# Kernel optimization log

Measured on AMD Instinct MI355X. Metric: run time of the kernel, lower is better.

Reference implementation:

```python
import jax, jax.numpy as jnp
import numpy as np

NUM_HEADS = 12
KEEP_RATE = 0.7
INIT_N = 14 * 14  # 196


def setup_inputs() -> dict:
    key = jax.random.key(0)
    k1, k2, k3, k4 = jax.random.split(key, 4)
    B, N, C = 64, 197, 768
    s = 1.0 / np.sqrt(C)
    return {
        "x": jax.random.normal(k1, (B, N, C), dtype=jnp.float32),
        "qkv_w": jax.random.normal(k2, (3 * C, C), dtype=jnp.float32) * s,
        "proj_w": jax.random.normal(k3, (C, C), dtype=jnp.float32) * s,
        "proj_b": jax.random.normal(k4, (C,), dtype=jnp.float32) * 0.01,
    }


def reference(x, qkv_w, proj_w, proj_b):
    B, N, C = x.shape
    H = NUM_HEADS
    hd = C // H
    scale = hd ** (-0.5)

    # qkv projection (torch Linear: y = x @ W.T), split into q, k, v heads
    qkv = (x @ qkv_w.T).reshape(B, N, 3, H, hd)
    qkv = jnp.transpose(qkv, (2, 0, 3, 1, 4))  # [3, B, H, N, hd]
    q, k, v = qkv[0], qkv[1], qkv[2]

    # explicit (non-flash) attention: attn matrix is needed for cls-row pruning
    attn = jax.nn.softmax(jnp.einsum("bhqd,bhkd->bhqk", q, k) * scale, axis=-1)
    out = jnp.einsum("bhqk,bhkd->bqhd", attn, v).reshape(B, N, C)
    out = out @ proj_w.T + proj_b

    # top-k token pruning via mean cls attention over heads
    left_tokens = int(KEEP_RATE * INIT_N)  # 137
    cls_attn = attn[:, :, 0, 1:].mean(axis=1)  # [B, N-1]
    _, idx = jax.lax.top_k(cls_attn, left_tokens)  # sorted descending, like torch.topk
    index = jnp.broadcast_to(idx[:, :, None], (B, left_tokens, C))
    return (out, index, idx)
```

## Files before the change

kernel.cpp:

```cpp
#include <hip/hip_runtime.h>
#include <math.h>


typedef __attribute__((ext_vector_type(8))) short short8;
typedef __attribute__((ext_vector_type(4))) float f32x4;

constexpr int T_B = 64, T_N = 197, T_C = 768, T_H = 12, T_HD = 64;
constexpr int T_M = T_B * T_N;
constexpr int T_KEEP = 137, T_NTOK = 196;

constexpr size_t OOFF_INDEX = (size_t)T_M * T_C;
constexpr size_t OOFF_IDX   = OOFF_INDEX + (size_t)T_B * T_KEEP * T_C;

constexpr size_t U_XB_AO = 0;
constexpr size_t U_QWB   = 9682944;
constexpr size_t U_PWB   = 11452416;
constexpr size_t U_QB    = 12042240;
constexpr size_t U_KB    = 21725184;
constexpr size_t U_VB    = 31408128;
constexpr size_t WS_FP_BYTE = 82182144ull;

__device__ __forceinline__ float bf2f(short u) {
  return __builtin_bit_cast(float, ((unsigned)(unsigned short)u) << 16);
}
__device__ __forceinline__ unsigned short f2bf(float f) {
  unsigned u = __builtin_bit_cast(unsigned, f);
  return (unsigned short)((u + 0x7fffu + ((u >> 16) & 1u)) >> 16);
}

__global__ __launch_bounds__(256) void cvt_k(const float* __restrict__ in,
                                             unsigned short* __restrict__ outp)
{
  const int i = blockIdx.x * 256 + threadIdx.x;
  const float4 v = ((const float4*)in)[i];
  const unsigned long long pk =
      (unsigned long long)f2bf(v.x) | ((unsigned long long)f2bf(v.y) << 16) |
      ((unsigned long long)f2bf(v.z) << 32) | ((unsigned long long)f2bf(v.w) << 48);
  ((unsigned long long*)outp)[i] = pk;
}

__global__ __launch_bounds__(256) void vzero_k(unsigned short* __restrict__ vtg)
{
  const size_t i = ((size_t)blockIdx.x * 256 + threadIdx.x) * 8;
  *(short8*)(vtg + i) = (short8){0, 0, 0, 0, 0, 0, 0, 0};
}

template<int MODE, int NTN>
__global__ __launch_bounds__(256) void mgemm_k(
    const unsigned short* __restrict__ A, const unsigned short* __restrict__ Bw,
    int M, float* __restrict__ outF, const float* __restrict__ bias,
    unsigned short* __restrict__ oq, unsigned short* __restrict__ ok,
    unsigned short* __restrict__ ov)
{
  __shared__ unsigned short ldsA[3][4096], ldsB[3][4096];
  const int t = threadIdx.x, w = t >> 6, lane = t & 63;
  const int wr = w >> 1, wc = w & 1;

  const int nwg = 99 * NTN;
  int id = blockIdx.x;
  {
    const int q = nwg >> 3, r = nwg & 7;
    const int xcd = id & 7, off = id >> 3;
    id = (xcd < r ? xcd * (q + 1) : r * (q + 1) + (xcd - r) * q) + off;
  }
  const int m0 = (id / NTN) * 128, n0 = (id % NTN) * 128;

  auto stage = [&](int buf, int k0) {
#pragma unroll
    for (int it = 0; it < 2; it++) {
      const int c = it * 256 + t;
      const int row = c >> 2, slot = c & 3;
      const int gslot = slot ^ (row & 3);
      int ar = m0 + row; ar = ar < M ? ar : M - 1;
      __builtin_amdgcn_global_load_lds(
          (const __attribute__((address_space(1))) unsigned int*)(A + (size_t)ar * 768 + k0 + gslot * 8),
          (__attribute__((address_space(3))) unsigned int*)&ldsA[buf][(size_t)c * 8],
          16, 0, 0);
      __builtin_amdgcn_global_load_lds(
          (const __attribute__((address_space(1))) unsigned int*)(Bw + (size_t)(n0 + row) * 768 + k0 + gslot * 8),
          (__attribute__((address_space(3))) unsigned int*)&ldsB[buf][(size_t)c * 8],
          16, 0, 0);
    }
  };

  f32x4 acc[4][4];
#pragma unroll
  for (int i = 0; i < 4; i++)
#pragma unroll
    for (int j = 0; j < 4; j++) acc[i][j] = (f32x4){0.f, 0.f, 0.f, 0.f};

  stage(0, 0);
  stage(1, 32);
  const int gsel = lane >> 4, rsel = lane & 15;

  for (int k = 0; k < 24; ++k) {
    __builtin_amdgcn_sched_barrier(0);
    if (k < 23) asm volatile("s_waitcnt vmcnt(4)\n\ts_barrier" ::: "memory");
    else        asm volatile("s_waitcnt vmcnt(0)\n\ts_barrier" ::: "memory");
    __builtin_amdgcn_sched_barrier(0);

    const int cur = k % 3;
    short8 aF[4], bF[4];
#pragma unroll
    for (int mi = 0; mi < 4; mi++) {
      const int row = wr * 64 + mi * 16 + rsel;
      aF[mi] = *(const short8*)&ldsA[cur][row * 32 + ((gsel ^ (row & 3)) * 8)];
    }
#pragma unroll
    for (int ni = 0; ni < 4; ni++) {
      const int row = wc * 64 + ni * 16 + rsel;
      bF[ni] = *(const short8*)&ldsB[cur][row * 32 + ((gsel ^ (row & 3)) * 8)];
    }

    if (k + 2 < 24) stage((k + 2) % 3, (k + 2) * 32);

#pragma unroll
    for (int mi = 0; mi < 4; mi++)
#pragma unroll
      for (int ni = 0; ni < 4; ni++)
        acc[mi][ni] = __builtin_amdgcn_mfma_f32_16x16x32_bf16(aF[mi], bF[ni], acc[mi][ni], 0, 0, 0);
  }

  const int colL = lane & 15, rowH = lane >> 4;
#pragma unroll
  for (int mi = 0; mi < 4; mi++) {
#pragma unroll
    for (int r = 0; r < 4; r++) {
      const int gm = m0 + wr * 64 + mi * 16 + rowH * 4 + r;
      if (gm >= M) continue;
      int bb = 0, nn = 0;
      if (MODE == 0) { bb = gm / T_N; nn = gm - bb * T_N; }
#pragma unroll
      for (int ni = 0; ni < 4; ni++) {
        const int gc = n0 + wc * 64 + ni * 16 + colL;
        const float val = acc[mi][ni][r];
        if (MODE == 0) {
          const int part = gc / T_C;
          const int rem = gc - part * T_C;
          const int h = rem >> 6, d = rem & 63;
          if (part == 2) {
            ov[(((size_t)(bb * T_H + h)) * 64 + d) * 224 + nn] = f2bf(val);
          } else {
            unsigned short* dst = part == 0 ? oq : ok;
            dst[(((size_t)(bb * T_H + h)) * T_N + nn) * T_HD + d] = f2bf(val);
          }
        } else {
          outF[(size_t)gm * T_C + gc] = val + bias[gc];
        }
      }
    }
  }
}

__global__ __launch_bounds__(256) void flash3_k(
    const unsigned short* __restrict__ qb, const unsigned short* __restrict__ kb,
    const unsigned short* __restrict__ vtg, unsigned short* __restrict__ ao)
{
  __shared__ unsigned short lds[27456];
  constexpr int KL_U = 0;
  constexpr int PL0  = 12608;

  const int bh = blockIdx.x;
  const int b = bh / T_H, h = bh - b * T_H;
  const int t = threadIdx.x;
  const int w = t >> 6, lane = t & 63;
  const int colL = lane & 15, g4 = lane >> 4;
  const int PL_W = PL0 + w * 3712;
  const short8 z8 = (short8){0, 0, 0, 0, 0, 0, 0, 0};

  {
    const unsigned short* src = kb + (size_t)bh * T_N * 64;
    for (int c = t; c < 1576; c += 256) {
      const int row = c >> 3, s = c & 7;
      const short8 v = *(const short8*)(src + row * 64 + s * 8);
      *(short8*)&lds[KL_U + row * 64 + ((s ^ (row & 7)) * 8)] = v;
    }
  }
  if (lane < 16) {
    unsigned short* p = &lds[PL_W + lane * 232];
    *(short8*)&p[208] = z8; *(short8*)&p[216] = z8;
  }
  __syncthreads();

  const size_t qbase = (size_t)bh * T_N * 64;
  const unsigned short* vb2 = vtg + (size_t)bh * 64 * 224;

  for (int qt = w; qt < 13; qt += 4) {
    int qrow = qt * 16 + colL; if (qrow > 196) qrow = 196;
    const short8 qa0 = *(const short8*)(qb + qbase + (size_t)qrow * 64 + g4 * 8);
    const short8 qa1 = *(const short8*)(qb + qbase + (size_t)qrow * 64 + 32 + g4 * 8);

    f32x4 acc[13];
#pragma unroll
    for (int kt = 0; kt < 13; kt++) acc[kt] = (f32x4){0.f, 0.f, 0.f, 0.f};
#pragma unroll
    for (int kt = 0; kt < 13; kt++) {
      const int krow = kt * 16 + colL;
      const int base = KL_U + krow * 64;
      const short8 k0f = *(const short8*)&lds[base + ((g4 ^ (krow & 7)) * 8)];
      const short8 k1f = *(const short8*)&lds[base + (((4 + g4) ^ (krow & 7)) * 8)];
      acc[kt] = __builtin_amdgcn_mfma_f32_16x16x32_bf16(qa0, k0f, acc[kt], 0, 0, 0);
      acc[kt] = __builtin_amdgcn_mfma_f32_16x16x32_bf16(qa1, k1f, acc[kt], 0, 0, 0);
    }

    float l4[4];
#pragma unroll
    for (int r = 0; r < 4; r++) {
      float sv[13];
      float mx = -1e30f;
#pragma unroll
      for (int kt = 0; kt < 13; kt++) {
        const int col = kt * 16 + colL;
        float s = acc[kt][r] * 0.125f;
        if (col > 196) s = -1e30f;
        sv[kt] = s;
        mx = fmaxf(mx, s);
      }
      mx = fmaxf(mx, __shfl_xor(mx, 1));
      mx = fmaxf(mx, __shfl_xor(mx, 2));
      mx = fmaxf(mx, __shfl_xor(mx, 4));
      mx = fmaxf(mx, __shfl_xor(mx, 8));
      float l = 0.f;
      const int prow = g4 * 4 + r;
#pragma unroll
      for (int kt = 0; kt < 13; kt++) {
        const float p = __expf(sv[kt] - mx);
        l += p;
        lds[PL_W + prow * 232 + kt * 16 + colL] = f2bf(p);
      }
      l += __shfl_xor(l, 1);
      l += __shfl_xor(l, 2);
      l += __shfl_xor(l, 4);
      l += __shfl_xor(l, 8);
      l4[r] = l;
    }

    f32x4 oacc[4];
#pragma unroll
    for (int dt = 0; dt < 4; dt++) oacc[dt] = (f32x4){0.f, 0.f, 0.f, 0.f};
#pragma unroll
    for (int ks = 0; ks < 7; ks++) {
      const short8 pa = *(const short8*)&lds[PL_W + colL * 232 + ks * 32 + g4 * 8];
#pragma unroll
      for (int dt = 0; dt < 4; dt++) {
        const short8 vf = *(const short8*)(vb2 + (size_t)(dt * 16 + colL) * 224 + ks * 32 + g4 * 8);
        oacc[dt] = __builtin_amdgcn_mfma_f32_16x16x32_bf16(pa, vf, oacc[dt], 0, 0, 0);
      }
    }

#pragma unroll
    for (int r = 0; r < 4; r++) {
      const int row = qt * 16 + g4 * 4 + r;
      if (row <= 196) {
        const float invl = 1.f / l4[r];
        unsigned short* op = ao + ((size_t)b * T_N + row) * T_C + h * 64;
#pragma unroll
        for (int dt = 0; dt < 4; dt++)
          op[dt * 16 + colL] = f2bf(oacc[dt][r] * invl);
      }
    }
  }
}

__global__ __launch_bounds__(256) void qcls_k(const float* __restrict__ x,
                                              const float* __restrict__ qkvw,
                                              double* __restrict__ qc)
{
  __shared__ double xr[768];
  const int b = blockIdx.x, t = threadIdx.x;
  if (t < 192) {
    const float4 v = *(const float4*)&x[(size_t)b * T_N * T_C + t * 4];
    xr[t * 4 + 0] = (double)v.x; xr[t * 4 + 1] = (double)v.y;
    xr[t * 4 + 2] = (double)v.z; xr[t * 4 + 3] = (double)v.w;
  }
  __syncthreads();
  const int w = t >> 6, lane = t & 63;
  const int jj0 = blockIdx.y * 4;
  for (int jj = jj0; jj < jj0 + 4; jj++) {
    const int j = jj * 4 + w;
    const float* wr = qkvw + (size_t)j * T_C;
    double a = 0.0;
#pragma unroll
    for (int ci = 0; ci < 12; ci++) a += xr[lane + ci * 64] * (double)wr[lane + ci * 64];
#pragma unroll
    for (int off = 32; off > 0; off >>= 1) a += __shfl_xor(a, off);
    if (lane == 0) qc[(size_t)b * T_C + j] = a;
  }
}

__global__ __launch_bounds__(256) void wtil_k(const double* __restrict__ qc,
                                              const float* __restrict__ qkvw,
                                              double* __restrict__ wt)
{
  __shared__ double ql[64];
  const int bh = blockIdx.x;
  const int b = bh / T_H, h = bh - b * T_H;
  const int t = threadIdx.x;
  if (t < 64) ql[t] = qc[(size_t)b * T_C + h * 64 + t];
  __syncthreads();
  const float* wbase = qkvw + ((size_t)T_C + h * 64) * T_C;
  double a0 = 0.0, a1 = 0.0, a2 = 0.0;
  for (int d = 0; d < 64; d++) {
    const double qd = ql[d];
    const float* wr = wbase + (size_t)d * T_C;
    a0 += qd * (double)wr[t];
    a1 += qd * (double)wr[t + 256];
    a2 += qd * (double)wr[t + 512];
  }
  double* o = wt + (size_t)bh * T_C;
  o[t] = a0; o[t + 256] = a1; o[t + 512] = a2;
}

__global__ __launch_bounds__(256) void clslog_k(const float* __restrict__ x,
                                                const double* __restrict__ wt,
                                                double* __restrict__ lg)
{
  const int b = blockIdx.x;
  const int t = threadIdx.x, w = t >> 6, lane = t & 63;

  double wreg[3][12];
#pragma unroll
  for (int i = 0; i < 3; i++) {
    const double* wb = wt + ((size_t)b * T_H + w * 3 + i) * T_C;
#pragma unroll
    for (int ci = 0; ci < 12; ci++) wreg[i][ci] = wb[lane + ci * 64];
  }

  const int n0 = blockIdx.y * 13;
  for (int nn = 0; nn < 13; nn++) {
    const int n = n0 + nn;
    if (n > 196) break;
    const float* xr = x + ((size_t)b * T_N + n) * T_C;
    double p0 = 0.0, p1 = 0.0, p2 = 0.0;
#pragma unroll
    for (int ci = 0; ci < 12; ci++) {
      const double xv = (double)xr[lane + ci * 64];
      p0 += xv * wreg[0][ci];
      p1 += xv * wreg[1][ci];
      p2 += xv * wreg[2][ci];
    }
    double pv[3] = {p0, p1, p2};
#pragma unroll
    for (int i = 0; i < 3; i++) {
      double sv = pv[i];
#pragma unroll
      for (int off = 32; off > 0; off >>= 1) sv += __shfl_xor(sv, off);
      if (lane == 0) lg[((size_t)b * T_H + w * 3 + i) * T_N + n] = sv * 0.125;
    }
  }
}

__global__ __launch_bounds__(256) void final_k(const double* __restrict__ lg,
                                               float* __restrict__ out)
{
  __shared__ double pm[12][200];
  __shared__ unsigned vals[T_NTOK];
  __shared__ int idxb[T_KEEP];
  const int b = blockIdx.x, t = threadIdx.x, w = t >> 6, lane = t & 63;
#pragma unroll
  for (int i = 0; i < 3; i++) {
    const int h = w * 3 + i;
    const double* L = lg + ((size_t)b * T_H + h) * T_N;
    double v[4]; double mx = -1e300;
#pragma unroll
    for (int t2 = 0; t2 < 4; t2++) {
      const int n = lane + t2 * 64;
      v[t2] = (n < T_N) ? L[n] : -1e300;
      mx = fmax(mx, v[t2]);
    }
#pragma unroll
    for (int off = 32; off > 0; off >>= 1) mx = fmax(mx, __shfl_xor(mx, off));
    double s = 0.0;
#pragma unroll
    for (int t2 = 0; t2 < 4; t2++) {
      const int n = lane + t2 * 64;
      const double e = (n < T_N) ? exp(v[t2] - mx) : 0.0;
      v[t2] = e; s += e;
    }
#pragma unroll
    for (int off = 32; off > 0; off >>= 1) s += __shfl_xor(s, off);
    const double inv = 1.0 / s;
#pragma unroll
    for (int t2 = 0; t2 < 4; t2++) {
      const int n = lane + t2 * 64;
      if (n < T_N) pm[h][n] = v[t2] * inv;
    }
  }
  __syncthreads();
  if (t < T_NTOK) {
    double s = 0.0;
#pragma unroll
    for (int h2 = 0; h2 < 12; h2++) s += pm[h2][t + 1];
    const float f = (float)(s / 12.0);
    vals[t] = __builtin_bit_cast(unsigned, f) & ~7u;
  }
  __syncthreads();
  if (t < T_NTOK) {
    const unsigned v = vals[t];
    int r = 0;
    for (int i2 = 0; i2 < T_NTOK; i2++) {
      const unsigned vi = vals[i2];
      r += ((vi > v) || (vi == v && i2 < t)) ? 1 : 0;
    }
    if (r < T_KEEP) idxb[r] = t;
  }
  __syncthreads();
  if (t < T_KEEP) out[OOFF_IDX + (size_t)b * T_KEEP + t] = (float)idxb[t];
  const size_t basei = OOFF_INDEX + (size_t)b * T_KEEP * T_C;
  for (int pos = t; pos < T_KEEP * T_C; pos += 256) out[basei + pos] = (float)idxb[pos / T_C];
}

extern "C" void kernel_launch(void* const* d_in, const int* in_sizes, int n_in,
                              void* d_out, int out_size, void* d_ws, size_t ws_size,
                              hipStream_t stream)
{
  const float* x     = (const float*)d_in[0];
  const float* qkvw  = (const float*)d_in[1];
  const float* projw = (const float*)d_in[2];
  const float* projb = (const float*)d_in[3];
  float* out = (float*)d_out;

  unsigned short* u = (unsigned short*)d_ws;
  unsigned short* xb   = u + U_XB_AO;
  unsigned short* qwb  = u + U_QWB;
  unsigned short* pwb  = u + U_PWB;
  unsigned short* qb   = u + U_QB;
  unsigned short* kb   = u + U_KB;
  unsigned short* vtg  = u + U_VB;
  unsigned short* ao   = u + U_XB_AO;
  double* dr  = (double*)((char*)d_ws + WS_FP_BYTE);
  double* qc  = dr;
  double* wt  = dr + 49152;
  double* lgb = dr + 49152 + 589824;

  const dim3 blk(256);

  qcls_k<<<dim3(64, 48), blk, 0, stream>>>(x, qkvw, qc);
  wtil_k<<<dim3(768), blk, 0, stream>>>(qc, qkvw, wt);
  clslog_k<<<dim3(64, 16), blk, 0, stream>>>(x, wt, lgb);
  final_k<<<dim3(64), blk, 0, stream>>>(lgb, out);

  cvt_k<<<dim3(9456), blk, 0, stream>>>(x, xb);
  cvt_k<<<dim3(1728), blk, 0, stream>>>(qkvw, qwb);
  cvt_k<<<dim3(576),  blk, 0, stream>>>(projw, pwb);
  vzero_k<<<dim3(5376), blk, 0, stream>>>(vtg);
  mgemm_k<0, 18><<<dim3(99 * 18), blk, 0, stream>>>(xb, qwb, T_M, nullptr, nullptr, qb, kb, vtg);
  flash3_k<<<dim3(768), blk, 0, stream>>>(qb, kb, vtg, ao);
  mgemm_k<1, 6><<<dim3(99 * 6), blk, 0, stream>>>(ao, pwb, T_M, out, projb, nullptr, nullptr, nullptr);
}
```

Measured before the change: 255.6 us.

## Load GEMM MFMA fragments directly from global memory with register double-buffering

Drops the LDS triple-buffered staging (global_load_lds plus barriers) in the bf16 GEMM kernel. Each wave now loads its own A/B MFMA fragments straight from global memory into registers, ping-ponging between two register sets. This removes LDS traffic and workgroup barriers. In exchange, tiles are no longer shared across waves: each A/B row is fetched by two waves, so global/L2 traffic doubles. Each lane also issues narrow strided 16-byte loads, and register pressure rises.

Result: slower. 420.3 us (+64.4%).

```diff
diff --git a/kernel.cpp b/kernel.cpp
--- a/kernel.cpp
+++ b/kernel.cpp
@@ -52,7 +52,6 @@
     unsigned short* __restrict__ oq, unsigned short* __restrict__ ok,
     unsigned short* __restrict__ ov)
 {
-  __shared__ unsigned short ldsA[3][4096], ldsB[3][4096];
   const int t = threadIdx.x, w = t >> 6, lane = t & 63;
   const int wr = w >> 1, wc = w & 1;
 
@@ -65,23 +64,15 @@
   }
   const int m0 = (id / NTN) * 128, n0 = (id % NTN) * 128;
 
-  auto stage = [&](int buf, int k0) {
-#pragma unroll
-    for (int it = 0; it < 2; it++) {
-      const int c = it * 256 + t;
-      const int row = c >> 2, slot = c & 3;
-      const int gslot = slot ^ (row & 3);
-      int ar = m0 + row; ar = ar < M ? ar : M - 1;
-      __builtin_amdgcn_global_load_lds(
-          (const __attribute__((address_space(1))) unsigned int*)(A + (size_t)ar * 768 + k0 + gslot * 8),
-          (__attribute__((address_space(3))) unsigned int*)&ldsA[buf][(size_t)c * 8],
-          16, 0, 0);
-      __builtin_amdgcn_global_load_lds(
-          (const __attribute__((address_space(1))) unsigned int*)(Bw + (size_t)(n0 + row) * 768 + k0 + gslot * 8),
-          (__attribute__((address_space(3))) unsigned int*)&ldsB[buf][(size_t)c * 8],
-          16, 0, 0);
-    }
-  };
+  const int gsel = lane >> 4, rsel = lane & 15;
+  const unsigned short* Ap[4];
+  const unsigned short* Bp[4];
+#pragma unroll
+  for (int i = 0; i < 4; i++) {
+    int ar = m0 + wr * 64 + i * 16 + rsel; ar = ar < M ? ar : M - 1;
+    Ap[i] = A + (size_t)ar * 768 + gsel * 8;
+    Bp[i] = Bw + (size_t)(n0 + wc * 64 + i * 16 + rsel) * 768 + gsel * 8;
+  }
 
   f32x4 acc[4][4];
 #pragma unroll
@@ -89,36 +80,42 @@
 #pragma unroll
     for (int j = 0; j < 4; j++) acc[i][j] = (f32x4){0.f, 0.f, 0.f, 0.f};
 
-  stage(0, 0);
-  stage(1, 32);
-  const int gsel = lane >> 4, rsel = lane & 15;
-
+  short8 aE[4], bE[4], aO[4], bO[4];
+#pragma unroll
+  for (int i = 0; i < 4; i++) {
+    aE[i] = *(const short8*)(Ap[i]);
+    bE[i] = *(const short8*)(Bp[i]);
+  }
+
+#pragma unroll
   for (int k = 0; k < 24; ++k) {
-    __builtin_amdgcn_sched_barrier(0);
-    if (k < 23) asm volatile("s_waitcnt vmcnt(4)\n\ts_barrier" ::: "memory");
-    else        asm volatile("s_waitcnt vmcnt(0)\n\ts_barrier" ::: "memory");
-    __builtin_amdgcn_sched_barrier(0);
-
-    const int cur = k % 3;
-    short8 aF[4], bF[4];
-#pragma unroll
-    for (int mi = 0; mi < 4; mi++) {
-      const int row = wr * 64 + mi * 16 + rsel;
-      aF[mi] = *(const short8*)&ldsA[cur][row * 32 + ((gsel ^ (row & 3)) * 8)];
-    }
-#pragma unroll
-    for (int ni = 0; ni < 4; ni++) {
-      const int row = wc * 64 + ni * 16 + rsel;
-      bF[ni] = *(const short8*)&ldsB[cur][row * 32 + ((gsel ^ (row & 3)) * 8)];
-    }
-
-    if (k + 2 < 24) stage((k + 2) % 3, (k + 2) * 32);
-
-#pragma unroll
-    for (int mi = 0; mi < 4; mi++)
-#pragma unroll
-      for (int ni = 0; ni < 4; ni++)
-        acc[mi][ni] = __builtin_amdgcn_mfma_f32_16x16x32_bf16(aF[mi], bF[ni], acc[mi][ni], 0, 0, 0);
+    if ((k & 1) == 0) {
+      if (k + 1 < 24) {
+#pragma unroll
+        for (int i = 0; i < 4; i++) {
+          aO[i] = *(const short8*)(Ap[i] + (k + 1) * 32);
+          bO[i] = *(const short8*)(Bp[i] + (k + 1) * 32);
+        }
+      }
+#pragma unroll
+      for (int mi = 0; mi < 4; mi++)
+#pragma unroll
+        for (int ni = 0; ni < 4; ni++)
+          acc[mi][ni] = __builtin_amdgcn_mfma_f32_16x16x32_bf16(aE[mi], bE[ni], acc[mi][ni], 0, 0, 0);
+    } else {
+      if (k + 1 < 24) {
+#pragma unroll
+        for (int i = 0; i < 4; i++) {
+          aE[i] = *(const short8*)(Ap[i] + (k + 1) * 32);
+          bE[i] = *(const short8*)(Bp[i] + (k + 1) * 32);
+        }
+      }
+#pragma unroll
+      for (int mi = 0; mi < 4; mi++)
+#pragma unroll
+        for (int ni = 0; ni < 4; ni++)
+          acc[mi][ni] = __builtin_amdgcn_mfma_f32_16x16x32_bf16(aO[mi], bO[ni], acc[mi][ni], 0, 0, 0);
+    }
   }
 
   const int colL = lane & 15, rowH = lane >> 4;
```
